# Optimization experiments

Hardware: AMD Instinct MI355X
Metric: run time of the kernel (lower is better)

## Reference

```python
import jax, jax.numpy as jnp
import numpy as np
import math

DIM = 1024
MAX_DEPTH = 16
ROPE_BASE = 10000.0
NUM_ACTIVE = 2

def setup_inputs() -> dict:
    key = jax.random.key(0)
    ks = jax.random.split(key, 6)
    bsz, seq, dim, E, hidden = 4, 1024, DIM, 8, 4 * DIM
    bound = 1.0 / math.sqrt(dim)
    return {
        "x": jax.random.normal(ks[0], (bsz, seq, dim), jnp.float32),
        "router_w": jax.random.normal(ks[1], (dim, dim), jnp.float32) * 0.02,
        "expert_keys": jax.random.uniform(ks[2], (E, dim), jnp.float32, -bound, bound),
        "expert_bias": jnp.zeros((E,), jnp.float32),
        "fc_w": jax.random.normal(ks[3], (E, hidden, dim), jnp.float32) * 0.02,
        "proj_w": jax.random.normal(ks[4], (E, dim, hidden), jnp.float32) * 0.02,
        "depth_idx": 3,
    }

def _rope_row(depth_idx, rev_idx, dtype):
    half = DIM // 2
    inv_freq = 1.0 / (ROPE_BASE ** (jnp.arange(0, DIM, 2, dtype=jnp.float32) / DIM))  # [half]
    f = depth_idx * inv_freq
    r = rev_idx * inv_freq
    return (jnp.cos(f).astype(dtype), jnp.sin(f).astype(dtype),
            jnp.cos(r).astype(dtype), jnp.sin(r).astype(dtype))

def reference(x, router_w, expert_keys, expert_bias, fc_w, proj_w, depth_idx):
    bsz, seq, dim = x.shape
    N = bsz * seq
    flat_x = x.reshape(N, dim)
    # router + RMSNorm (no weight, eps = machine eps, matching F.rms_norm default)
    q = flat_x @ router_w.T
    eps = jnp.asarray(jnp.finfo(q.dtype).eps, q.dtype)
    q = q * jax.lax.rsqrt(jnp.mean(q * q, axis=-1, keepdims=True) + eps)
    # depth RoPE (forward freq on first half pairing, reverse freq on second half)
    half = dim // 2
    cos, sin, rcos, rsin = _rope_row(float(depth_idx), float(MAX_DEPTH - 1 - depth_idx), q.dtype)
    q1, q2 = q[..., :half], q[..., half:]
    q = jnp.concatenate((q1 * cos + q2 * sin, -q1 * rsin + q2 * rcos), axis=-1)
    # routing
    logits = (q @ expert_keys.T) / math.sqrt(dim)  # [N, E]
    gate_values = jax.nn.sigmoid(logits)
    biased = logits + expert_bias
    _, topk_idx = jax.lax.top_k(biased, NUM_ACTIVE)  # [N, k]
    topk_gates = jnp.take_along_axis(gate_values, topk_idx, axis=-1)
    topk_gates = topk_gates / jnp.clip(topk_gates.sum(-1, keepdims=True), 1e-9, None)
    gates = jnp.zeros_like(gate_values).at[jnp.arange(N)[:, None], topk_idx].set(topk_gates)
    # dense all-expert MLP: relu(x W_fc^T)^2 W_proj^T, then mask-and-sum
    h = jax.nn.relu(jnp.einsum('nd,ehd->neh', flat_x, fc_w))
    expert_out = jnp.einsum('neh,edh->ned', h * h, proj_w)  # [N, E, dim]
    y = jnp.einsum('ned,ne->nd', expert_out, gates)
    return y.reshape(bsz, seq, dim)
```

## Files before the change

kernel.cpp:

```cpp
#include <hip/hip_runtime.h>
#include <hip/hip_bf16.h>
#include <math.h>

#define N_TOK 4096
#define DIM_V 1024
#define NEXP  8
#define HID   4096
#define NSLOT 9216

typedef short  s16x8 __attribute__((ext_vector_type(8)));
typedef unsigned short u16x8 __attribute__((ext_vector_type(8)));
typedef unsigned short u16x4 __attribute__((ext_vector_type(4)));
typedef float  f32x4 __attribute__((ext_vector_type(4)));

constexpr size_t OFF_XB   = 0;
constexpr size_t OFF_WB   = OFF_XB + 8388608;
constexpr size_t OFF_RK   = OFF_WB + 2097152;
constexpr size_t OFF_KPP  = OFF_RK + 65536;
constexpr size_t OFF_SSQ  = OFF_KPP + 65536;
constexpr size_t OFF_CNT  = OFF_SSQ + 16384;
constexpr size_t OFF_CUR  = OFF_CNT + 128;
constexpr size_t OFF_TOK  = OFF_CUR + 128;
constexpr size_t OFF_GSL  = OFF_TOK + 36864;
constexpr size_t ZERO_BEG = OFF_KPP;
constexpr size_t ZERO_END = OFF_GSL + 36864;
constexpr size_t OFF_OFFP = ZERO_END;
constexpr size_t OFF_IDX2 = OFF_OFFP + 128;
constexpr size_t OFF_G2   = OFF_IDX2 + 32768;
constexpr size_t OFF_INV  = OFF_G2 + 32768;
constexpr size_t SMALL_END = OFF_INV + 32768;

constexpr size_t A_OFF_FCB = SMALL_END;
constexpr size_t A_OFF_PO  = A_OFF_FCB;
constexpr size_t A_OFF_PJB = A_OFF_FCB + 67108864;
constexpr size_t A_OFF_H2  = A_OFF_PJB + 67108864;
constexpr size_t WS_FULL   = A_OFF_H2 + 75497472;

__device__ inline unsigned short f2bf(float f) {
  __hip_bfloat16 h = __float2bfloat16(f);
  return __builtin_bit_cast(unsigned short, h);
}

__device__ __forceinline__ void gload16(const void* g, void* l) {
  __builtin_amdgcn_global_load_lds(
      (const __attribute__((address_space(1))) unsigned int*)g,
      (__attribute__((address_space(3))) unsigned int*)l, 16, 0, 0);
}

__global__ __launch_bounds__(256) void k_cvt_all(
    const float* __restrict__ x, const float* __restrict__ rw,
    const float* __restrict__ fw, const float* __restrict__ pw,
    unsigned short* __restrict__ xb, unsigned short* __restrict__ wb,
    unsigned short* __restrict__ fcb, unsigned short* __restrict__ pjb) {
  constexpr int E0 = (N_TOK * DIM_V) / 4096;
  constexpr int E1 = E0 + (DIM_V * DIM_V) / 4096;
  constexpr int E2 = E1 + (NEXP * HID * DIM_V) / 4096;
  constexpr int E3 = E2 + (NEXP * HID * DIM_V) / 4096;
  constexpr int UPB = 8;
  int u = (int)blockIdx.x * UPB;
  const int uend = u + UPB;
  while (u < uend) {
    const f32x4* s; u16x4* d; int ru0, rend;
    if (u < E0)      { s = (const f32x4*)x;  d = (u16x4*)xb;  ru0 = 0;  rend = E0; }
    else if (u < E1) { s = (const f32x4*)rw; d = (u16x4*)wb;  ru0 = E0; rend = E1; }
    else if (u < E2) { s = (const f32x4*)fw; d = (u16x4*)fcb; ru0 = E1; rend = E2; }
    else             { s = (const f32x4*)pw; d = (u16x4*)pjb; ru0 = E2; rend = E3; }
    const int span = (uend < rend ? uend : rend) - u;
    int j = (u - ru0) * 1024 + (int)threadIdx.x;
#pragma unroll 2
    for (int k = 0; k < span; ++k, j += 1024) {
      f32x4 v0 = __builtin_nontemporal_load(s + j);
      f32x4 v1 = __builtin_nontemporal_load(s + j + 256);
      f32x4 v2 = __builtin_nontemporal_load(s + j + 512);
      f32x4 v3 = __builtin_nontemporal_load(s + j + 768);
      u16x4 o0 = { f2bf(v0.x), f2bf(v0.y), f2bf(v0.z), f2bf(v0.w) };
      u16x4 o1 = { f2bf(v1.x), f2bf(v1.y), f2bf(v1.z), f2bf(v1.w) };
      u16x4 o2 = { f2bf(v2.x), f2bf(v2.y), f2bf(v2.z), f2bf(v2.w) };
      u16x4 o3 = { f2bf(v3.x), f2bf(v3.y), f2bf(v3.z), f2bf(v3.w) };
      __builtin_nontemporal_store(o0, d + j);
      __builtin_nontemporal_store(o1, d + j + 256);
      __builtin_nontemporal_store(o2, d + j + 512);
      __builtin_nontemporal_store(o3, d + j + 768);
    }
    u += span;
  }
}

__global__ __launch_bounds__(256) void k_colsum(const float* __restrict__ W,
                                                const float* __restrict__ keys,
                                                const int* __restrict__ depth,
                                                double* __restrict__ kpp) {
  __shared__ double rks[NEXP][64];
  const int d0 = blockIdx.y * 64;
  const int t = threadIdx.x;
  if (t < 64) {
    const int d = d0 + t;
    const int dep = depth[0];
    const bool lower = d < 512;
    const int i = lower ? d : d - 512;
    double p = pow(10000.0, (double)i / 512.0);
    float invf = 1.0f / (float)p;
    float ff = (float)dep * invf;
    float rr = (float)(15 - dep) * invf;
    float cf  = (float)cos((double)ff);
    float sf  = (float)sin((double)ff);
    float rcf = (float)cos((double)rr);
    float rsf = (float)sin((double)rr);
    for (int e = 0; e < NEXP; ++e) {
      double k1 = (double)keys[e * DIM_V + i];
      double k2 = (double)keys[e * DIM_V + 512 + i];
      rks[e][t] = lower ? ((double)cf * k1 - (double)rsf * k2)
                        : ((double)sf * k1 + (double)rcf * k2);
    }
  }
  __syncthreads();
  const int j = blockIdx.x * 256 + t;
  double acc[NEXP] = {};
  for (int dd = 0; dd < 64; ++dd) {
    double w = (double)W[(size_t)(d0 + dd) * DIM_V + j];
#pragma unroll
    for (int e = 0; e < NEXP; ++e) acc[e] += w * rks[e][dd];
  }
  for (int e = 0; e < NEXP; ++e) atomicAdd(&kpp[e * DIM_V + j], acc[e]);
}

__global__ __launch_bounds__(256) void k_gate(const float* __restrict__ x,
                                              const double* __restrict__ kpp,
                                              const float* __restrict__ sumsq,
                                              const float* __restrict__ bias,
                                              int* __restrict__ idx2, float* __restrict__ gates2,
                                              int* __restrict__ counts) {
  int wave = (blockIdx.x * 256 + threadIdx.x) >> 6;
  int lane = threadIdx.x & 63;
  if (wave >= N_TOK) return;
  const float4* xr = (const float4*)(x + (size_t)wave * DIM_V);
  double a[NEXP] = {};
#pragma unroll
  for (int j = 0; j < 4; ++j) {
    int c = lane + 64 * j;
    float4 v = xr[c];
#pragma unroll
    for (int e = 0; e < NEXP; ++e) {
      const double* kp = kpp + (size_t)e * DIM_V + c * 4;
      a[e] += (double)v.x * kp[0] + (double)v.y * kp[1] +
              (double)v.z * kp[2] + (double)v.w * kp[3];
    }
  }
#pragma unroll
  for (int e = 0; e < NEXP; ++e)
    for (int d = 1; d < 64; d <<= 1) a[e] += __shfl_xor(a[e], d, 64);
  if (lane == 0) {
    float s = rsqrtf(sumsq[wave] * (1.0f / 1024.0f) + 1.1920928955078125e-7f);
    float z[NEXP], b[NEXP];
#pragma unroll
    for (int e = 0; e < NEXP; ++e) {
      z[e] = (float)(a[e] * (double)s * (1.0 / 32.0));
      b[e] = z[e] + bias[e];
    }
    int i1 = 0;
    for (int e = 1; e < NEXP; ++e) if (b[e] > b[i1]) i1 = e;
    int i2 = -1;
    for (int e = 0; e < NEXP; ++e) if (e != i1 && (i2 < 0 || b[e] > b[i2])) i2 = e;
    float g1 = 1.f / (1.f + expf(-z[i1]));
    float g2 = 1.f / (1.f + expf(-z[i2]));
    float sm = fmaxf(g1 + g2, 1e-9f);
    idx2[wave * 2] = i1; idx2[wave * 2 + 1] = i2;
    gates2[wave * 2] = g1 / sm; gates2[wave * 2 + 1] = g2 / sm;
    atomicAdd(&counts[i1], 1); atomicAdd(&counts[i2], 1);
  }
}

__global__ void k_scatter(const int* __restrict__ idx2, const float* __restrict__ gates2,
                          const int* __restrict__ counts, int* __restrict__ cursor,
                          int* __restrict__ tok, float* __restrict__ gsl,
                          int* __restrict__ inv, int* __restrict__ offp_out) {
  int off[NEXP + 1];
  off[0] = 0;
  for (int e = 0; e < NEXP; ++e) off[e + 1] = off[e] + ((counts[e] + 127) & ~127);
  int n = blockIdx.x * 256 + threadIdx.x;
  if (blockIdx.x == 0 && threadIdx.x == 0)
    for (int e = 0; e <= NEXP; ++e) offp_out[e] = off[e];
  if (n >= N_TOK) return;
  for (int r = 0; r < 2; ++r) {
    int e = idx2[n * 2 + r];
    int pos = atomicAdd(&cursor[e], 1);
    int slot = off[e] + pos;
    tok[slot] = n; gsl[slot] = gates2[n * 2 + r]; inv[n * 2 + r] = slot;
  }
}

__global__ __launch_bounds__(256) void k_qt(
    const unsigned short* __restrict__ Aptr,
    const unsigned short* __restrict__ Wptr,
    float* __restrict__ sumsq) {
  constexpr int KD = DIM_V;
  constexpr int GNB = DIM_V / 128;
  constexpr int NT  = KD / 64;
  const int G = gridDim.x, q = G >> 3;
  const int idp = ((int)blockIdx.x & 7) * q + ((int)blockIdx.x >> 3);
  const int n0 = (idp % GNB) * 128, m0 = (idp / GNB) * 128;
  const unsigned short* Bp = Wptr + (size_t)n0 * KD;

  __shared__ alignas(16) char smem[65536];
  const int tid = threadIdx.x, wid = tid >> 6, lane = tid & 63;
  const int wr = (wid >> 1) * 64, wc = (wid & 1) * 64;
  const int rql  = tid >> 3;
  const int swc8 = ((tid & 7) ^ ((tid >> 3) & 7)) * 8;
  const int frow = lane & 15, fsl = lane >> 4, fkey = lane & 7;

  auto stage = [&](int k0s, unsigned db) {
#pragma unroll
    for (int p = 0; p < 4; ++p)
      gload16(Aptr + (size_t)(m0 + p * 32 + rql) * KD + k0s + swc8,
              smem + db + p * 4096 + wid * 1024);
#pragma unroll
    for (int p = 0; p < 4; ++p)
      gload16(Bp + (size_t)(p * 32 + rql) * KD + k0s + swc8,
              smem + db + 16384 + p * 4096 + wid * 1024);
  };

  f32x4 acc[4][4] = {};
  stage(0, 0);
#pragma unroll 2
  for (int t = 0; t < NT; ++t) {
    int tn = t + 1; if (tn == NT) tn = 0;
    stage(tn * 64, (unsigned)((t + 1) & 1) * 32768u);
    asm volatile("s_waitcnt vmcnt(8)" ::: "memory");
    __builtin_amdgcn_s_barrier();
    __builtin_amdgcn_sched_barrier(0);
    const unsigned Ab = (unsigned)(t & 1) * 32768u, Bb = Ab + 16384u;
    s16x8 af[2][4], bfr[2][4];
#pragma unroll
    for (int kk2 = 0; kk2 < 2; ++kk2) {
      const unsigned so = (unsigned)(((fsl + kk2 * 4) ^ fkey) << 4);
#pragma unroll
      for (int m = 0; m < 4; ++m)
        af[kk2][m] = *(const s16x8*)(smem + Ab + (unsigned)(wr + m * 16 + frow) * 128 + so);
#pragma unroll
      for (int n = 0; n < 4; ++n)
        bfr[kk2][n] = *(const s16x8*)(smem + Bb + (unsigned)(wc + n * 16 + frow) * 128 + so);
    }
    __builtin_amdgcn_s_setprio(1);
#pragma unroll
    for (int kk2 = 0; kk2 < 2; ++kk2)
#pragma unroll
      for (int m = 0; m < 4; ++m)
#pragma unroll
        for (int n = 0; n < 4; ++n)
          acc[m][n] = __builtin_amdgcn_mfma_f32_16x16x32_bf16(af[kk2][m], bfr[kk2][n],
                                                              acc[m][n], 0, 0, 0);
    __builtin_amdgcn_s_setprio(0);
    __builtin_amdgcn_sched_barrier(0);
    __builtin_amdgcn_s_barrier();
  }

#pragma unroll
  for (int m = 0; m < 4; ++m)
#pragma unroll
    for (int j = 0; j < 4; ++j) {
      const int grow = m0 + wr + m * 16 + (lane >> 4) * 4 + j;
      float s = 0.f;
#pragma unroll
      for (int n = 0; n < 4; ++n) { float v = acc[m][n][j]; s += v * v; }
      s += __shfl_xor(s, 1, 64); s += __shfl_xor(s, 2, 64);
      s += __shfl_xor(s, 4, 64); s += __shfl_xor(s, 8, 64);
      if ((lane & 15) == 0) atomicAdd(&sumsq[grow], s);
    }
}

__global__ __launch_bounds__(512) void k_fc256(
    const unsigned short* __restrict__ xb,
    const unsigned short* __restrict__ fcb,
    const int* __restrict__ offp, const int* __restrict__ tok,
    unsigned short* __restrict__ h2) {
  constexpr int KD = DIM_V;
  constexpr int NT = KD / 64;
  const int G = gridDim.x, q = G >> 3;
  const int idp = ((int)blockIdx.x & 7) * q + ((int)blockIdx.x >> 3);
  const int bx = idp >> 4;
  const int n0 = (idp & 15) * 256;
  int c = 0, e = 0, m0 = -1;
  for (e = 0; e < NEXP; ++e) {
    int nb = (offp[e + 1] - offp[e] + 255) >> 8;
    if (bx < c + nb) { m0 = offp[e] + (bx - c) * 256; break; }
    c += nb;
  }
  if (m0 < 0) return;
  const int segend = offp[e + 1];
  const unsigned short* Bp = fcb + ((size_t)e * HID + n0) * KD;

  __shared__ alignas(16) char smem[131072];
  const int tid = threadIdx.x, wid = tid >> 6, lane = tid & 63;
  const int wr = (wid >> 2) * 128, wcc = (wid & 3) * 64;
  const int swc8 = ((tid & 7) ^ ((tid >> 3) & 7)) * 8;
  const int frow = lane & 15, fsl = lane >> 4, fkey = lane & 7;

  int arow[4];
#pragma unroll
  for (int p = 0; p < 4; ++p) {
    int rr = m0 + p * 64 + (tid >> 3);
    arow[p] = tok[rr < NSLOT ? rr : NSLOT - 1];
  }

  auto stage = [&](int k0s, unsigned db) {
#pragma unroll
    for (int p = 0; p < 4; ++p)
      gload16(xb + (size_t)arow[p] * KD + k0s + swc8,
              smem + db + p * 8192 + wid * 1024);
#pragma unroll
    for (int p = 0; p < 4; ++p)
      gload16(Bp + (size_t)(p * 64 + (tid >> 3)) * KD + k0s + swc8,
              smem + db + 32768 + p * 8192 + wid * 1024);
  };

  f32x4 acc[8][4] = {};
  stage(0, 0);
  for (int t = 0; t < NT; ++t) {
    int tn = t + 1; if (tn == NT) tn = 0;
    stage(tn * 64, (unsigned)((t + 1) & 1) * 65536u);
    asm volatile("s_waitcnt vmcnt(8)" ::: "memory");
    __builtin_amdgcn_s_barrier();
    __builtin_amdgcn_sched_barrier(0);
    const unsigned Ab = (unsigned)(t & 1) * 65536u, Bb = Ab + 32768u;
#pragma unroll
    for (int kk2 = 0; kk2 < 2; ++kk2) {
      const unsigned so = (unsigned)(((fsl + kk2 * 4) ^ fkey) << 4);
      s16x8 af[8], bfr[4];
#pragma unroll
      for (int m = 0; m < 8; ++m)
        af[m] = *(const s16x8*)(smem + Ab + (unsigned)(wr + m * 16 + frow) * 128 + so);
#pragma unroll
      for (int n = 0; n < 4; ++n)
        bfr[n] = *(const s16x8*)(smem + Bb + (unsigned)(wcc + n * 16 + frow) * 128 + so);
      __builtin_amdgcn_s_setprio(1);
#pragma unroll
      for (int m = 0; m < 8; ++m)
#pragma unroll
        for (int n = 0; n < 4; ++n)
          acc[m][n] = __builtin_amdgcn_mfma_f32_16x16x32_bf16(af[m], bfr[n], acc[m][n], 0, 0, 0);
      __builtin_amdgcn_s_setprio(0);
    }
    __builtin_amdgcn_sched_barrier(0);
    __builtin_amdgcn_s_barrier();
  }
#pragma unroll
  for (int m = 0; m < 8; ++m)
#pragma unroll
    for (int j = 0; j < 4; ++j) {
      const int grow = m0 + wr + m * 16 + (lane >> 4) * 4 + j;
      if (grow < segend) {
#pragma unroll
        for (int n = 0; n < 4; ++n) {
          float v = acc[m][n][j];
          v = v > 0.f ? v * v : 0.f;
          h2[(size_t)grow * HID + n0 + wcc + n * 16 + (lane & 15)] = f2bf(v);
        }
      }
    }
}

__global__ __launch_bounds__(256) void k_proj(
    const unsigned short* __restrict__ h2,
    const unsigned short* __restrict__ pjb,
    const int* __restrict__ offp, const float* __restrict__ gsl,
    float* __restrict__ po) {
  constexpr int KD  = HID;
  constexpr int GNB = DIM_V / 128;
  constexpr int NT  = KD / 64;
  const int G = gridDim.x, q = G >> 3;
  const int idp = ((int)blockIdx.x & 7) * q + ((int)blockIdx.x >> 3);
  const int n0 = (idp % GNB) * 128, m0 = (idp / GNB) * 128;
  if (m0 >= offp[NEXP]) return;
  int e = 0; while (e < NEXP - 1 && m0 >= offp[e + 1]) ++e;
  const unsigned short* Bp = pjb + ((size_t)e * DIM_V + n0) * KD;

  __shared__ alignas(16) char smem[65536];
  const int tid = threadIdx.x, wid = tid >> 6, lane = tid & 63;
  const int wr = (wid >> 1) * 64, wc = (wid & 1) * 64;
  const int rql  = tid >> 3;
  const int swc8 = ((tid & 7) ^ ((tid >> 3) & 7)) * 8;
  const int frow = lane & 15, fsl = lane >> 4, fkey = lane & 7;

  auto stage = [&](int k0s, unsigned db) {
#pragma unroll
    for (int p = 0; p < 4; ++p)
      gload16(h2 + (size_t)(m0 + p * 32 + rql) * KD + k0s + swc8,
              smem + db + p * 4096 + wid * 1024);
#pragma unroll
    for (int p = 0; p < 4; ++p)
      gload16(Bp + (size_t)(p * 32 + rql) * KD + k0s + swc8,
              smem + db + 16384 + p * 4096 + wid * 1024);
  };

  f32x4 acc[4][4] = {};
  stage(0, 0);
#pragma unroll 2
  for (int t = 0; t < NT; ++t) {
    int tn = t + 1; if (tn == NT) tn = 0;
    stage(tn * 64, (unsigned)((t + 1) & 1) * 32768u);
    asm volatile("s_waitcnt vmcnt(8)" ::: "memory");
    __builtin_amdgcn_s_barrier();
    __builtin_amdgcn_sched_barrier(0);
    const unsigned Ab = (unsigned)(t & 1) * 32768u, Bb = Ab + 16384u;
    s16x8 af[2][4], bfr[2][4];
#pragma unroll
    for (int kk2 = 0; kk2 < 2; ++kk2) {
      const unsigned so = (unsigned)(((fsl + kk2 * 4) ^ fkey) << 4);
#pragma unroll
      for (int m = 0; m < 4; ++m)
        af[kk2][m] = *(const s16x8*)(smem + Ab + (unsigned)(wr + m * 16 + frow) * 128 + so);
#pragma unroll
      for (int n = 0; n < 4; ++n)
        bfr[kk2][n] = *(const s16x8*)(smem + Bb + (unsigned)(wc + n * 16 + frow) * 128 + so);
    }
    __builtin_amdgcn_s_setprio(1);
#pragma unroll
    for (int kk2 = 0; kk2 < 2; ++kk2)
#pragma unroll
      for (int m = 0; m < 4; ++m)
#pragma unroll
        for (int n = 0; n < 4; ++n)
          acc[m][n] = __builtin_amdgcn_mfma_f32_16x16x32_bf16(af[kk2][m], bfr[kk2][n],
                                                              acc[m][n], 0, 0, 0);
    __builtin_amdgcn_s_setprio(0);
    __builtin_amdgcn_sched_barrier(0);
    __builtin_amdgcn_s_barrier();
  }

#pragma unroll
  for (int m = 0; m < 4; ++m)
#pragma unroll
    for (int j = 0; j < 4; ++j) {
      const int grow = m0 + wr + m * 16 + (lane >> 4) * 4 + j;
      const float g = gsl[grow];
#pragma unroll
      for (int n = 0; n < 4; ++n)
        po[(size_t)grow * DIM_V + n0 + wc + n * 16 + (lane & 15)] = acc[m][n][j] * g;
    }
}

__global__ void k_combine(const float* __restrict__ po, const int* __restrict__ inv,
                          float* __restrict__ y) {
  const int total = N_TOK * (DIM_V / 4);
  for (int i = blockIdx.x * blockDim.x + threadIdx.x; i < total;
       i += gridDim.x * blockDim.x) {
    int n = i >> 8, c = i & 255;
    int s1 = inv[n * 2], s2 = inv[n * 2 + 1];
    float4 a = ((const float4*)(po + (size_t)s1 * DIM_V))[c];
    float4 b = ((const float4*)(po + (size_t)s2 * DIM_V))[c];
    float4 o; o.x = a.x + b.x; o.y = a.y + b.y; o.z = a.z + b.z; o.w = a.w + b.w;
    ((float4*)(y + (size_t)n * DIM_V))[c] = o;
  }
}

extern "C" void kernel_launch(void* const* d_in, const int* in_sizes, int n_in,
                              void* d_out, int out_size, void* d_ws, size_t ws_size,
                              hipStream_t stream) {
  if (ws_size < WS_FULL) return;
  const float* x      = (const float*)d_in[0];
  const float* rw     = (const float*)d_in[1];
  const float* keys   = (const float*)d_in[2];
  const float* bias   = (const float*)d_in[3];
  const float* fc_w   = (const float*)d_in[4];
  const float* proj_w = (const float*)d_in[5];
  const int*   depth  = (const int*)d_in[6];
  char* ws = (char*)d_ws;
  unsigned short* xb  = (unsigned short*)(ws + OFF_XB);
  unsigned short* wb  = (unsigned short*)(ws + OFF_WB);
  double* kpp   = (double*)(ws + OFF_KPP);
  float*  ssq   = (float*)(ws + OFF_SSQ);
  int*    cnt   = (int*)(ws + OFF_CNT);
  int*    cur   = (int*)(ws + OFF_CUR);
  int*    tok   = (int*)(ws + OFF_TOK);
  float*  gsl   = (float*)(ws + OFF_GSL);
  int*    offp  = (int*)(ws + OFF_OFFP);
  int*    idx2  = (int*)(ws + OFF_IDX2);
  float*  g2    = (float*)(ws + OFF_G2);
  int*    inv   = (int*)(ws + OFF_INV);
  unsigned short* fcb = (unsigned short*)(ws + A_OFF_FCB);
  unsigned short* pjb = (unsigned short*)(ws + A_OFF_PJB);
  unsigned short* h2  = (unsigned short*)(ws + A_OFF_H2);
  float*  po    = (float*)(ws + A_OFF_PO);
  float*  y     = (float*)d_out;

  hipMemsetAsync(ws + ZERO_BEG, 0, ZERO_END - ZERO_BEG, stream);
  k_cvt_all<<<2208, 256, 0, stream>>>(x, rw, fc_w, proj_w, xb, wb, fcb, pjb);
  k_colsum<<<dim3(4, 16), 256, 0, stream>>>(rw, keys, depth, kpp);
  k_qt<<<dim3(32 * 8), 256, 0, stream>>>(xb, wb, ssq);
  k_gate<<<1024, 256, 0, stream>>>(x, kpp, ssq, bias, idx2, g2, cnt);
  k_scatter<<<16, 256, 0, stream>>>(idx2, g2, cnt, cur, tok, gsl, inv, offp);
  k_fc256<<<dim3(44 * 16), 512, 0, stream>>>(xb, fcb, offp, tok, h2);
  k_proj<<<dim3(72 * 8), 256, 0, stream>>>(h2, pjb, offp, gsl, po);
  k_combine<<<2048, 256, 0, stream>>>(po, inv, y);
}
```

Baseline: 458.9 us.

## Merge router GEMM, key projection and expert weight conversion into one launch

Splits the conversion kernel so that only x and the router weight are converted first. The router sum-of-squares GEMM, the rotated-key column-sum, and the large fc/proj weight bf16 conversion then run as disjoint block ranges of a single kernel. The aim is to overlap the compute-bound router GEMM with the bandwidth-bound weight conversion and to drop two launches. The cost is that every block now reserves 64KB of shared memory, including the conversion blocks, which may reduce occupancy for the conversion work.

```diff
diff --git a/kernel.cpp b/kernel.cpp
--- a/kernel.cpp
+++ b/kernel.cpp
@@ -47,28 +47,153 @@
       (__attribute__((address_space(3))) unsigned int*)l, 16, 0, 0);
 }
 
-__global__ __launch_bounds__(256) void k_cvt_all(
+__global__ __launch_bounds__(256) void k_cvt_xw(
     const float* __restrict__ x, const float* __restrict__ rw,
+    unsigned short* __restrict__ xb, unsigned short* __restrict__ wb) {
+  int u = (int)blockIdx.x * 8;
+  const f32x4* s; u16x4* d; int base;
+  if (u < 1024) { s = (const f32x4*)x;  d = (u16x4*)xb; base = u; }
+  else          { s = (const f32x4*)rw; d = (u16x4*)wb; base = u - 1024; }
+  int j = base * 1024 + (int)threadIdx.x;
+#pragma unroll 2
+  for (int k = 0; k < 8; ++k, j += 1024) {
+    f32x4 v0 = __builtin_nontemporal_load(s + j);
+    f32x4 v1 = __builtin_nontemporal_load(s + j + 256);
+    f32x4 v2 = __builtin_nontemporal_load(s + j + 512);
+    f32x4 v3 = __builtin_nontemporal_load(s + j + 768);
+    u16x4 o0 = { f2bf(v0.x), f2bf(v0.y), f2bf(v0.z), f2bf(v0.w) };
+    u16x4 o1 = { f2bf(v1.x), f2bf(v1.y), f2bf(v1.z), f2bf(v1.w) };
+    u16x4 o2 = { f2bf(v2.x), f2bf(v2.y), f2bf(v2.z), f2bf(v2.w) };
+    u16x4 o3 = { f2bf(v3.x), f2bf(v3.y), f2bf(v3.z), f2bf(v3.w) };
+    __builtin_nontemporal_store(o0, d + j);
+    __builtin_nontemporal_store(o1, d + j + 256);
+    __builtin_nontemporal_store(o2, d + j + 512);
+    __builtin_nontemporal_store(o3, d + j + 768);
+  }
+}
+
+constexpr int QTG = 256, CSG = 64, CVG = 2048;
+
+__global__ __launch_bounds__(256) void k_mega(
+    const unsigned short* __restrict__ xb, const unsigned short* __restrict__ wb,
+    float* __restrict__ sumsq,
+    const float* __restrict__ W, const float* __restrict__ keys,
+    const int* __restrict__ depth, double* __restrict__ kpp,
     const float* __restrict__ fw, const float* __restrict__ pw,
-    unsigned short* __restrict__ xb, unsigned short* __restrict__ wb,
     unsigned short* __restrict__ fcb, unsigned short* __restrict__ pjb) {
-  constexpr int E0 = (N_TOK * DIM_V) / 4096;
-  constexpr int E1 = E0 + (DIM_V * DIM_V) / 4096;
-  constexpr int E2 = E1 + (NEXP * HID * DIM_V) / 4096;
-  constexpr int E3 = E2 + (NEXP * HID * DIM_V) / 4096;
-  constexpr int UPB = 8;
-  int u = (int)blockIdx.x * UPB;
-  const int uend = u + UPB;
-  while (u < uend) {
-    const f32x4* s; u16x4* d; int ru0, rend;
-    if (u < E0)      { s = (const f32x4*)x;  d = (u16x4*)xb;  ru0 = 0;  rend = E0; }
-    else if (u < E1) { s = (const f32x4*)rw; d = (u16x4*)wb;  ru0 = E0; rend = E1; }
-    else if (u < E2) { s = (const f32x4*)fw; d = (u16x4*)fcb; ru0 = E1; rend = E2; }
-    else             { s = (const f32x4*)pw; d = (u16x4*)pjb; ru0 = E2; rend = E3; }
-    const int span = (uend < rend ? uend : rend) - u;
-    int j = (u - ru0) * 1024 + (int)threadIdx.x;
+  __shared__ alignas(16) char smem[65536];
+  const int bid = (int)blockIdx.x;
+  const int tid = threadIdx.x;
+
+  if (bid < QTG) {
+    constexpr int KD = DIM_V, GNB = DIM_V / 128, NT = KD / 64, q = QTG >> 3;
+    const int idp = (bid & 7) * q + (bid >> 3);
+    const int n0 = (idp % GNB) * 128, m0 = (idp / GNB) * 128;
+    const unsigned short* Bp = wb + (size_t)n0 * KD;
+    const int wid = tid >> 6, lane = tid & 63;
+    const int wr = (wid >> 1) * 64, wc = (wid & 1) * 64;
+    const int rql  = tid >> 3;
+    const int swc8 = ((tid & 7) ^ ((tid >> 3) & 7)) * 8;
+    const int frow = lane & 15, fsl = lane >> 4, fkey = lane & 7;
+
+    auto stage = [&](int k0s, unsigned db) {
+#pragma unroll
+      for (int p = 0; p < 4; ++p)
+        gload16(xb + (size_t)(m0 + p * 32 + rql) * KD + k0s + swc8,
+                smem + db + p * 4096 + wid * 1024);
+#pragma unroll
+      for (int p = 0; p < 4; ++p)
+        gload16(Bp + (size_t)(p * 32 + rql) * KD + k0s + swc8,
+                smem + db + 16384 + p * 4096 + wid * 1024);
+    };
+
+    f32x4 acc[4][4] = {};
+    stage(0, 0);
 #pragma unroll 2
-    for (int k = 0; k < span; ++k, j += 1024) {
+    for (int t = 0; t < NT; ++t) {
+      int tn = t + 1; if (tn == NT) tn = 0;
+      stage(tn * 64, (unsigned)((t + 1) & 1) * 32768u);
+      asm volatile("s_waitcnt vmcnt(8)" ::: "memory");
+      __builtin_amdgcn_s_barrier();
+      __builtin_amdgcn_sched_barrier(0);
+      const unsigned Ab = (unsigned)(t & 1) * 32768u, Bb = Ab + 16384u;
+      s16x8 af[2][4], bfr[2][4];
+#pragma unroll
+      for (int kk2 = 0; kk2 < 2; ++kk2) {
+        const unsigned so = (unsigned)(((fsl + kk2 * 4) ^ fkey) << 4);
+#pragma unroll
+        for (int m = 0; m < 4; ++m)
+          af[kk2][m] = *(const s16x8*)(smem + Ab + (unsigned)(wr + m * 16 + frow) * 128 + so);
+#pragma unroll
+        for (int n = 0; n < 4; ++n)
+          bfr[kk2][n] = *(const s16x8*)(smem + Bb + (unsigned)(wc + n * 16 + frow) * 128 + so);
+      }
+      __builtin_amdgcn_s_setprio(1);
+#pragma unroll
+      for (int kk2 = 0; kk2 < 2; ++kk2)
+#pragma unroll
+        for (int m = 0; m < 4; ++m)
+#pragma unroll
+          for (int n = 0; n < 4; ++n)
+            acc[m][n] = __builtin_amdgcn_mfma_f32_16x16x32_bf16(af[kk2][m], bfr[kk2][n],
+                                                                acc[m][n], 0, 0, 0);
+      __builtin_amdgcn_s_setprio(0);
+      __builtin_amdgcn_sched_barrier(0);
+      __builtin_amdgcn_s_barrier();
+    }
+#pragma unroll
+    for (int m = 0; m < 4; ++m)
+#pragma unroll
+      for (int j = 0; j < 4; ++j) {
+        const int grow = m0 + wr + m * 16 + (lane >> 4) * 4 + j;
+        float s = 0.f;
+#pragma unroll
+        for (int n = 0; n < 4; ++n) { float v = acc[m][n][j]; s += v * v; }
+        s += __shfl_xor(s, 1, 64); s += __shfl_xor(s, 2, 64);
+        s += __shfl_xor(s, 4, 64); s += __shfl_xor(s, 8, 64);
+        if ((lane & 15) == 0) atomicAdd(&sumsq[grow], s);
+      }
+  } else if (bid < QTG + CSG) {
+    double (*rks)[64] = (double(*)[64])smem;
+    const int cid = bid - QTG;
+    const int d0 = (cid >> 2) * 64;
+    if (tid < 64) {
+      const int d = d0 + tid;
+      const int dep = depth[0];
+      const bool lower = d < 512;
+      const int i = lower ? d : d - 512;
+      double p = pow(10000.0, (double)i / 512.0);
+      float invf = 1.0f / (float)p;
+      float ff = (float)dep * invf;
+      float rr = (float)(15 - dep) * invf;
+      float cf  = (float)cos((double)ff);
+      float sf  = (float)sin((double)ff);
+      float rcf = (float)cos((double)rr);
+      float rsf = (float)sin((double)rr);
+      for (int e = 0; e < NEXP; ++e) {
+        double k1 = (double)keys[e * DIM_V + i];
+        double k2 = (double)keys[e * DIM_V + 512 + i];
+        rks[e][tid] = lower ? ((double)cf * k1 - (double)rsf * k2)
+                            : ((double)sf * k1 + (double)rcf * k2);
+      }
+    }
+    __syncthreads();
+    const int j = (cid & 3) * 256 + tid;
+    double acc[NEXP] = {};
+    for (int dd = 0; dd < 64; ++dd) {
+      double w = (double)W[(size_t)(d0 + dd) * DIM_V + j];
+#pragma unroll
+      for (int e = 0; e < NEXP; ++e) acc[e] += w * rks[e][dd];
+    }
+    for (int e = 0; e < NEXP; ++e) atomicAdd(&kpp[e * DIM_V + j], acc[e]);
+  } else {
+    int u = (bid - QTG - CSG) * 8;
+    const f32x4* s; u16x4* d; int base;
+    if (u < 8192) { s = (const f32x4*)fw; d = (u16x4*)fcb; base = u; }
+    else          { s = (const f32x4*)pw; d = (u16x4*)pjb; base = u - 8192; }
+    int j = base * 1024 + tid;
+#pragma unroll 2
+    for (int k = 0; k < 8; ++k, j += 1024) {
       f32x4 v0 = __builtin_nontemporal_load(s + j);
       f32x4 v1 = __builtin_nontemporal_load(s + j + 256);
       f32x4 v2 = __builtin_nontemporal_load(s + j + 512);
@@ -82,46 +207,7 @@
       __builtin_nontemporal_store(o2, d + j + 512);
       __builtin_nontemporal_store(o3, d + j + 768);
     }
-    u += span;
-  }
-}
-
-__global__ __launch_bounds__(256) void k_colsum(const float* __restrict__ W,
-                                                const float* __restrict__ keys,
-                                                const int* __restrict__ depth,
-                                                double* __restrict__ kpp) {
-  __shared__ double rks[NEXP][64];
-  const int d0 = blockIdx.y * 64;
-  const int t = threadIdx.x;
-  if (t < 64) {
-    const int d = d0 + t;
-    const int dep = depth[0];
-    const bool lower = d < 512;
-    const int i = lower ? d : d - 512;
-    double p = pow(10000.0, (double)i / 512.0);
-    float invf = 1.0f / (float)p;
-    float ff = (float)dep * invf;
-    float rr = (float)(15 - dep) * invf;
-    float cf  = (float)cos((double)ff);
-    float sf  = (float)sin((double)ff);
-    float rcf = (float)cos((double)rr);
-    float rsf = (float)sin((double)rr);
-    for (int e = 0; e < NEXP; ++e) {
-      double k1 = (double)keys[e * DIM_V + i];
-      double k2 = (double)keys[e * DIM_V + 512 + i];
-      rks[e][t] = lower ? ((double)cf * k1 - (double)rsf * k2)
-                        : ((double)sf * k1 + (double)rcf * k2);
-    }
-  }
-  __syncthreads();
-  const int j = blockIdx.x * 256 + t;
-  double acc[NEXP] = {};
-  for (int dd = 0; dd < 64; ++dd) {
-    double w = (double)W[(size_t)(d0 + dd) * DIM_V + j];
-#pragma unroll
-    for (int e = 0; e < NEXP; ++e) acc[e] += w * rks[e][dd];
-  }
-  for (int e = 0; e < NEXP; ++e) atomicAdd(&kpp[e * DIM_V + j], acc[e]);
+  }
 }
 
 __global__ __launch_bounds__(256) void k_gate(const float* __restrict__ x,
@@ -187,85 +273,6 @@
     int slot = off[e] + pos;
     tok[slot] = n; gsl[slot] = gates2[n * 2 + r]; inv[n * 2 + r] = slot;
   }
-}
-
-__global__ __launch_bounds__(256) void k_qt(
-    const unsigned short* __restrict__ Aptr,
-    const unsigned short* __restrict__ Wptr,
-    float* __restrict__ sumsq) {
-  constexpr int KD = DIM_V;
-  constexpr int GNB = DIM_V / 128;
-  constexpr int NT  = KD / 64;
-  const int G = gridDim.x, q = G >> 3;
-  const int idp = ((int)blockIdx.x & 7) * q + ((int)blockIdx.x >> 3);
-  const int n0 = (idp % GNB) * 128, m0 = (idp / GNB) * 128;
-  const unsigned short* Bp = Wptr + (size_t)n0 * KD;
-
-  __shared__ alignas(16) char smem[65536];
-  const int tid = threadIdx.x, wid = tid >> 6, lane = tid & 63;
-  const int wr = (wid >> 1) * 64, wc = (wid & 1) * 64;
-  const int rql  = tid >> 3;
-  const int swc8 = ((tid & 7) ^ ((tid >> 3) & 7)) * 8;
-  const int frow = lane & 15, fsl = lane >> 4, fkey = lane & 7;
-
-  auto stage = [&](int k0s, unsigned db) {
-#pragma unroll
-    for (int p = 0; p < 4; ++p)
-      gload16(Aptr + (size_t)(m0 + p * 32 + rql) * KD + k0s + swc8,
-              smem + db + p * 4096 + wid * 1024);
-#pragma unroll
-    for (int p = 0; p < 4; ++p)
-      gload16(Bp + (size_t)(p * 32 + rql) * KD + k0s + swc8,
-              smem + db + 16384 + p * 4096 + wid * 1024);
-  };
-
-  f32x4 acc[4][4] = {};
-  stage(0, 0);
-#pragma unroll 2
-  for (int t = 0; t < NT; ++t) {
-    int tn = t + 1; if (tn == NT) tn = 0;
-    stage(tn * 64, (unsigned)((t + 1) & 1) * 32768u);
-    asm volatile("s_waitcnt vmcnt(8)" ::: "memory");
-    __builtin_amdgcn_s_barrier();
-    __builtin_amdgcn_sched_barrier(0);
-    const unsigned Ab = (unsigned)(t & 1) * 32768u, Bb = Ab + 16384u;
-    s16x8 af[2][4], bfr[2][4];
-#pragma unroll
-    for (int kk2 = 0; kk2 < 2; ++kk2) {
-      const unsigned so = (unsigned)(((fsl + kk2 * 4) ^ fkey) << 4);
-#pragma unroll
-      for (int m = 0; m < 4; ++m)
-        af[kk2][m] = *(const s16x8*)(smem + Ab + (unsigned)(wr + m * 16 + frow) * 128 + so);
-#pragma unroll
-      for (int n = 0; n < 4; ++n)
-        bfr[kk2][n] = *(const s16x8*)(smem + Bb + (unsigned)(wc + n * 16 + frow) * 128 + so);
-    }
-    __builtin_amdgcn_s_setprio(1);
-#pragma unroll
-    for (int kk2 = 0; kk2 < 2; ++kk2)
-#pragma unroll
-      for (int m = 0; m < 4; ++m)
-#pragma unroll
-        for (int n = 0; n < 4; ++n)
-          acc[m][n] = __builtin_amdgcn_mfma_f32_16x16x32_bf16(af[kk2][m], bfr[kk2][n],
-                                                              acc[m][n], 0, 0, 0);
-    __builtin_amdgcn_s_setprio(0);
-    __builtin_amdgcn_sched_barrier(0);
-    __builtin_amdgcn_s_barrier();
-  }
-
-#pragma unroll
-  for (int m = 0; m < 4; ++m)
-#pragma unroll
-    for (int j = 0; j < 4; ++j) {
-      const int grow = m0 + wr + m * 16 + (lane >> 4) * 4 + j;
-      float s = 0.f;
-#pragma unroll
-      for (int n = 0; n < 4; ++n) { float v = acc[m][n][j]; s += v * v; }
-      s += __shfl_xor(s, 1, 64); s += __shfl_xor(s, 2, 64);
-      s += __shfl_xor(s, 4, 64); s += __shfl_xor(s, 8, 64);
-      if ((lane & 15) == 0) atomicAdd(&sumsq[grow], s);
-    }
 }
 
 __global__ __launch_bounds__(512) void k_fc256(
@@ -484,9 +491,9 @@
   float*  y     = (float*)d_out;
 
   hipMemsetAsync(ws + ZERO_BEG, 0, ZERO_END - ZERO_BEG, stream);
-  k_cvt_all<<<2208, 256, 0, stream>>>(x, rw, fc_w, proj_w, xb, wb, fcb, pjb);
-  k_colsum<<<dim3(4, 16), 256, 0, stream>>>(rw, keys, depth, kpp);
-  k_qt<<<dim3(32 * 8), 256, 0, stream>>>(xb, wb, ssq);
+  k_cvt_xw<<<160, 256, 0, stream>>>(x, rw, xb, wb);
+  k_mega<<<QTG + CSG + CVG, 256, 0, stream>>>(xb, wb, ssq, rw, keys, depth, kpp,
+                                              fc_w, proj_w, fcb, pjb);
   k_gate<<<1024, 256, 0, stream>>>(x, kpp, ssq, bias, idx2, g2, cnt);
   k_scatter<<<16, 256, 0, stream>>>(idx2, g2, cnt, cur, tok, gsl, inv, offp);
   k_fc256<<<dim3(44 * 16), 512, 0, stream>>>(xb, fcb, offp, tok, h2);
```

Measured after the change: 437.2 us (median of 2 runs). -4.7%, faster.
